# Performance work log

Hardware: AMD Instinct MI355X
Metric: run time of the kernel (lower is better)

Reference implementation:

```python
import jax, jax.numpy as jnp
import numpy as np

COMMITMENT_COST = 0.25
ENTROPY_LOSS_RATIO = 0.1
ENTROPY_TEMPERATURE = 0.01


def setup_inputs() -> dict:
    key = jax.random.key(0)
    k1, k2 = jax.random.split(key)
    x = jax.random.normal(k1, (64, 32, 32, 256), dtype=jnp.float32)
    # variance_scaling(fan_in, uniform) init for the codebook parameter
    codebook_size, emb_dim = 1024, 256
    limit = jnp.sqrt(3.0 / emb_dim)
    codebook = jax.random.uniform(k2, (codebook_size, emb_dim), jnp.float32, -limit, limit)
    return {"x": x, "codebook": codebook}


def _squared_euclidean_distance(a, b):
    # a: (n, d), b: (m, d) -> (n, m)
    a2 = jnp.sum(a * a, axis=1, keepdims=True)          # (n, 1)
    b2 = jnp.sum(b * b, axis=1)[None, :]                # (1, m)
    ab = jnp.matmul(a, b.T)                             # (n, m)
    return a2 - 2.0 * ab + b2


def _entropy_loss(affinity, temperature):
    # affinity: (..., K); loss_type='softmax'
    flat = affinity.reshape(-1, affinity.shape[-1]) / temperature
    probs = jax.nn.softmax(flat, axis=-1)
    log_probs = jax.nn.log_softmax(flat + 1e-05, axis=-1)
    target_probs = probs
    avg_probs = jnp.mean(target_probs, axis=0)
    avg_entropy = -jnp.sum(avg_probs * jnp.log(avg_probs + 1e-05))
    sample_entropy = -jnp.mean(jnp.sum(target_probs * log_probs, axis=-1))
    return sample_entropy - avg_entropy


def reference(x, codebook):
    sg = jax.lax.stop_gradient
    emb_dim = x.shape[-1]
    codebook_size = codebook.shape[0]
    flat_x = x.reshape(-1, emb_dim)                              # (N, d)
    distances = _squared_euclidean_distance(flat_x, codebook)    # (N, K)
    distances = distances.reshape(x.shape[:-1] + (codebook_size,))
    encoding_indices = jnp.argmin(distances, axis=-1)            # (B,H,W) int
    # quantize: onehot @ codebook == gather of codebook rows
    quantized = jnp.take(codebook, encoding_indices, axis=0)     # (B,H,W,d)

    e_latent_loss = jnp.mean((sg(quantized) - x) ** 2) * COMMITMENT_COST
    q_latent_loss = jnp.mean((quantized - sg(x)) ** 2)
    entropy_loss = _entropy_loss(-distances, ENTROPY_TEMPERATURE) * ENTROPY_LOSS_RATIO
    loss = (e_latent_loss + q_latent_loss + entropy_loss).astype(jnp.float32)

    # straight-through estimator
    quantized = x + sg(quantized - x)
    return quantized, loss, encoding_indices
```

## Files before the change

kernel.cpp:

```cpp
#include <hip/hip_runtime.h>
#include <math.h>

#define NROWS 65536
#define DIM   256
#define KCB   1024
#define TM    32
#define NBLK  (NROWS / TM)
#define QOFF  (NROWS * DIM)
#define IDXOFF (QOFF + 1)

#define WS_DMIN 0
#define WS_PLP  1
#define WS_AVGP 4
#define WS_C2   (WS_AVGP + 8 * 1024)
#define WS_CBF  (WS_C2 + 1024)

#define DELTA 0.05f
#define XBP   264

typedef __attribute__((ext_vector_type(8))) __bf16 bf16x8;
typedef __attribute__((ext_vector_type(4))) float  f32x4;
typedef __attribute__((ext_vector_type(8))) unsigned short u16x8;
typedef __attribute__((ext_vector_type(4))) unsigned short u16x4;

#define EP_REDD 0
#define EP_REDK 256
#define EP_RT1  512
#define EP_RT2  768
#define EP_GMIN 1024
#define EP_CNT  1056
#define EP_CAND 1088
#define EP_CEX  1600
#define EP_R1F  2112
#define EP_SP   2144
#define EP_KFIN 2176
#define EP_DFIN 2208
#define EP_AVGP 2240
#define EP_SIZE 3264

__device__ __forceinline__ unsigned short f2bf(float f) {
    unsigned u = __float_as_uint(f);
    u += 0x7fffu + ((u >> 16) & 1u);
    return (unsigned short)(u >> 16);
}

__global__ __launch_bounds__(256) void prep_kernel(const float* __restrict__ cb,
                                                   float* __restrict__ ws) {
    int gid = blockIdx.x * 256 + threadIdx.x;
    if (gid < 4) ws[gid] = 0.f;
    if (gid < 8192) ws[WS_AVGP + gid] = 0.f;

    int k  = gid >> 5;
    int s  = gid & 31;
    int kc = s >> 2;
    int qq = s & 3;

    if (gid < 1024) {
        const float4* row = (const float4*)(cb + (size_t)gid * DIM);
        float ssum = 0.f;
#pragma unroll 8
        for (int i = 0; i < DIM / 4; ++i) {
            float4 v = row[i];
            ssum += v.x * v.x + v.y * v.y + v.z * v.z + v.w * v.w;
        }
        ws[WS_C2 + gid] = ssum;
    }

    unsigned short* cbf = (unsigned short*)(ws + WS_CBF);
    const float* src = cb + (size_t)k * DIM + (kc << 5) + (qq << 3);
    float4 v0 = *(const float4*)src, v1 = *(const float4*)(src + 4);
    u16x8 o;
    o[0] = f2bf(v0.x); o[1] = f2bf(v0.y); o[2] = f2bf(v0.z); o[3] = f2bf(v0.w);
    o[4] = f2bf(v1.x); o[5] = f2bf(v1.y); o[6] = f2bf(v1.z); o[7] = f2bf(v1.w);
    *(u16x8*)(cbf + ((((size_t)(kc << 10) + k) << 2) + qq) * 8) = o;
}

__global__ __launch_bounds__(512, 4) void vq_main(const float* __restrict__ x,
                                                  const float* __restrict__ cb,
                                                  float* __restrict__ ws,
                                                  float* __restrict__ out) {
    __shared__ float epi[EP_SIZE];
    __shared__ unsigned short xs[32 * XBP];

    const int tid  = threadIdx.x;
    const int w    = tid >> 6;
    const int lane = tid & 63;
    const int m    = lane & 15;
    const int q    = lane >> 4;
    const int R0   = blockIdx.x * TM;

    const u16x8* cbf = (const u16x8*)(ws + WS_CBF);
    const u16x8* bbase = cbf + (((w << 6) + m) << 2) + q;

    u16x8 breg[2][4];
    bf16x8 ah[2];

    float4 t0 = *((const float4*)(x + (size_t)(R0 + (w << 2) + 0) * DIM) + lane);
    float4 t1 = *((const float4*)(x + (size_t)(R0 + (w << 2) + 1) * DIM) + lane);
    float4 t2 = *((const float4*)(x + (size_t)(R0 + (w << 2) + 2) * DIM) + lane);
    float4 t3 = *((const float4*)(x + (size_t)(R0 + (w << 2) + 3) * DIM) + lane);

    {
        const u16x8* p = bbase;
        breg[0][0] = p[0]; breg[0][1] = p[64]; breg[0][2] = p[128]; breg[0][3] = p[192];
    }

    {
        u16x4 o;
        o[0] = f2bf(t0.x); o[1] = f2bf(t0.y); o[2] = f2bf(t0.z); o[3] = f2bf(t0.w);
        *(u16x4*)(xs + ((w << 2) + 0) * XBP + (lane << 2)) = o;
        o[0] = f2bf(t1.x); o[1] = f2bf(t1.y); o[2] = f2bf(t1.z); o[3] = f2bf(t1.w);
        *(u16x4*)(xs + ((w << 2) + 1) * XBP + (lane << 2)) = o;
        o[0] = f2bf(t2.x); o[1] = f2bf(t2.y); o[2] = f2bf(t2.z); o[3] = f2bf(t2.w);
        *(u16x4*)(xs + ((w << 2) + 2) * XBP + (lane << 2)) = o;
        o[0] = f2bf(t3.x); o[1] = f2bf(t3.y); o[2] = f2bf(t3.z); o[3] = f2bf(t3.w);
        *(u16x4*)(xs + ((w << 2) + 3) * XBP + (lane << 2)) = o;
    }

    f32x4 acc[2][8];
#pragma unroll
    for (int a = 0; a < 2; ++a)
#pragma unroll
        for (int b = 0; b < 8; ++b) acc[a][b] = (f32x4)0.f;

    __syncthreads();

    ah[0] = __builtin_bit_cast(bf16x8, *(const u16x8*)(xs + m * XBP + (q << 3)));
    ah[1] = __builtin_bit_cast(bf16x8, *(const u16x8*)(xs + (16 + m) * XBP + (q << 3)));

#pragma unroll
    for (int sub = 0; sub < 16; ++sub) {
        const int pb = sub & 1;
        if (sub < 15) {
            const int ns = sub + 1;
            const u16x8* p = bbase + ((ns >> 1) << 12) + ((ns & 1) << 11);
            breg[pb ^ 1][0] = p[0];   breg[pb ^ 1][1] = p[64];
            breg[pb ^ 1][2] = p[128]; breg[pb ^ 1][3] = p[192];
        }
#pragma unroll
        for (int ct = 0; ct < 4; ++ct) {
            bf16x8 bh = __builtin_bit_cast(bf16x8, breg[pb][ct]);
            int cg = ((sub & 1) << 2) + ct;
            acc[0][cg] = __builtin_amdgcn_mfma_f32_16x16x32_bf16(ah[0], bh, acc[0][cg], 0, 0, 0);
            acc[1][cg] = __builtin_amdgcn_mfma_f32_16x16x32_bf16(ah[1], bh, acc[1][cg], 0, 0, 0);
        }
        if ((sub & 1) == 1 && sub < 15) {
            const int nkc = (sub >> 1) + 1;
            ah[0] = __builtin_bit_cast(bf16x8, *(const u16x8*)(xs + m * XBP + (nkc << 5) + (q << 3)));
            ah[1] = __builtin_bit_cast(bf16x8, *(const u16x8*)(xs + (16 + m) * XBP + (nkc << 5) + (q << 3)));
        }
    }

    if (tid < 32) ((int*)(epi + EP_CNT))[tid] = 0;
#pragma unroll
    for (int t = tid; t < 1024; t += 512) epi[EP_AVGP + t] = 0.f;

    float c2v[8];
#pragma unroll
    for (int cg = 0; cg < 8; ++cg) {
        int col = ((cg >> 2) << 9) + (w << 6) + ((cg & 3) << 4) + m;
        c2v[cg] = ws[WS_C2 + col];
    }
#pragma unroll
    for (int rt = 0; rt < 2; ++rt) {
#pragma unroll
        for (int reg = 0; reg < 4; ++reg) {
            int row = (rt << 4) + (q << 2) + reg;
            float md = 3.0e38f; int mk = 0;
#pragma unroll
            for (int cg = 0; cg < 8; ++cg) {
                float g = c2v[cg] - 2.0f * acc[rt][cg][reg];
                acc[rt][cg][reg] = g;
                int col = ((cg >> 2) << 9) + (w << 6) + ((cg & 3) << 4) + m;
                if (g < md) { md = g; mk = col; }
            }
#pragma unroll
            for (int off = 1; off <= 8; off <<= 1) {
                float od = __shfl_xor(md, off, 64);
                int   ok = __shfl_xor(mk, off, 64);
                if (od < md || (od == md && ok < mk)) { md = od; mk = ok; }
            }
            if (m == 0) {
                epi[EP_REDD + (w << 5) + row] = md;
                ((int*)(epi + EP_REDK))[(w << 5) + row] = mk;
            }
        }
    }
    __syncthreads();

    if (tid < 32) {
        float gm = 3.0e38f;
#pragma unroll
        for (int wv = 0; wv < 8; ++wv) {
            float d = epi[EP_REDD + (wv << 5) + tid];
            if (d < gm) gm = d;
        }
        epi[EP_GMIN + tid] = gm;
    }
    __syncthreads();

    {
        int* cnt  = (int*)(epi + EP_CNT);
        int* cand = (int*)(epi + EP_CAND);
#pragma unroll
        for (int rt = 0; rt < 2; ++rt) {
#pragma unroll
            for (int reg = 0; reg < 4; ++reg) {
                int row = (rt << 4) + (q << 2) + reg;
                float gm = epi[EP_GMIN + row];
                float t1 = 0.f, t2 = 0.f;
#pragma unroll
                for (int cg = 0; cg < 8; ++cg) {
                    float g = acc[rt][cg][reg];
                    if (g < gm + DELTA) {
                        int col = ((cg >> 2) << 9) + (w << 6) + ((cg & 3) << 4) + m;
                        int pos = atomicAdd(&cnt[row], 1);
                        if (pos < 16) cand[(row << 4) + pos] = col;
                    }
                    float z = -100.0f * (g - gm);
                    float e = __expf(z);
                    acc[rt][cg][reg] = e;
                    t1 += e;
                    t2 += e * z;
                }
#pragma unroll
                for (int off = 1; off <= 8; off <<= 1) {
                    t1 += __shfl_xor(t1, off, 64);
                    t2 += __shfl_xor(t2, off, 64);
                }
                if (m == 0) {
                    epi[EP_RT1 + (w << 5) + row] = t1;
                    epi[EP_RT2 + (w << 5) + row] = t2;
                }
            }
        }
    }
    __syncthreads();

    if (tid < 32) {
        float T1 = 0.f, T2 = 0.f;
#pragma unroll
        for (int wv = 0; wv < 8; ++wv) {
            T1 += epi[EP_RT1 + (wv << 5) + tid];
            T2 += epi[EP_RT2 + (wv << 5) + tid];
        }
        float r1 = 1.0f / T1;
        epi[EP_R1F + tid] = r1;
        epi[EP_SP + tid]  = T2 * r1 - logf(T1);
    }
    __syncthreads();

    {
        float r1v[2][4];
#pragma unroll
        for (int rt = 0; rt < 2; ++rt)
#pragma unroll
            for (int reg = 0; reg < 4; ++reg)
                r1v[rt][reg] = epi[EP_R1F + (rt << 4) + (q << 2) + reg];
#pragma unroll
        for (int cg = 0; cg < 8; ++cg) {
            float s = 0.f;
#pragma unroll
            for (int rt = 0; rt < 2; ++rt)
#pragma unroll
                for (int reg = 0; reg < 4; ++reg)
                    s += acc[rt][cg][reg] * r1v[rt][reg];
            s += __shfl_xor(s, 16, 64);
            s += __shfl_xor(s, 32, 64);
            if (lane < 16) {
                int col = ((cg >> 2) << 9) + (w << 6) + ((cg & 3) << 4) + m;
                epi[EP_AVGP + col] += s;
            }
        }
    }
    {
        int* cnt  = (int*)(epi + EP_CNT);
        int* cand = (int*)(epi + EP_CAND);
        int r = tid >> 4;
        int i = tid & 15;
        int n = cnt[r]; if (n > 16) n = 16;
        if (i < n) {
            int k = cand[(r << 4) + i];
            const float4* ax = (const float4*)(x  + (((size_t)(R0 + r)) << 8));
            const float4* bx = (const float4*)(cb + (((size_t)k) << 8));
            float ab = 0.f, x2 = 0.f;
#pragma unroll 8
            for (int d4 = 0; d4 < 64; ++d4) {
                float4 a = ax[d4], b = bx[d4];
                ab = fmaf(a.x, b.x, ab);
                ab = fmaf(a.y, b.y, ab);
                ab = fmaf(a.z, b.z, ab);
                ab = fmaf(a.w, b.w, ab);
                x2 += a.x * a.x + a.y * a.y + a.z * a.z + a.w * a.w;
            }
            float t = 2.0f * ab;
            epi[EP_CEX + (r << 4) + i] = (x2 - t) + ws[WS_C2 + k];
        }
    }
    __syncthreads();

    if (tid < 32) {
        int* cnt  = (int*)(epi + EP_CNT);
        int* cand = (int*)(epi + EP_CAND);
        int n = cnt[tid]; if (n > 16) n = 16;
        float bd = epi[EP_CEX + (tid << 4)];
        int   bk = cand[(tid << 4)];
        for (int i = 1; i < n; ++i) {
            float d = epi[EP_CEX + (tid << 4) + i];
            int   k = cand[(tid << 4) + i];
            if (d < bd || (d == bd && k < bk)) { bd = d; bk = k; }
        }
        ((int*)(epi + EP_KFIN))[tid] = bk;
        epi[EP_DFIN + tid] = bd;
        out[IDXOFF + R0 + tid] = (float)bk;
    }
    __syncthreads();

#pragma unroll
    for (int rr = 0; rr < 4; ++rr) {
        int r = (w << 2) + rr;
        int k = ((int*)(epi + EP_KFIN))[r];
        f32x4 v = *((const f32x4*)(cb + (((size_t)k) << 8)) + lane);
        __builtin_nontemporal_store(v, (f32x4*)(out + (((size_t)(R0 + r)) << 8)) + lane);
    }
    for (int t = tid; t < 1024; t += 512)
        atomicAdd(ws + WS_AVGP + ((blockIdx.x & 7) << 10) + t, epi[EP_AVGP + t]);
    if (tid < 32) {
        float sp = epi[EP_SP + tid];
        float dd = epi[EP_DFIN + tid];
#pragma unroll
        for (int off = 1; off <= 16; off <<= 1) {
            sp += __shfl_xor(sp, off, 64);
            dd += __shfl_xor(dd, off, 64);
        }
        if (tid == 0) {
            atomicAdd(ws + WS_PLP, sp);
            atomicAdd(ws + WS_DMIN, dd);
        }
    }
}

__global__ __launch_bounds__(256) void vq_finalize(const float* __restrict__ ws,
                                                   float* __restrict__ out) {
    __shared__ float red[4];
    int tid = threadIdx.x;
    float part = 0.f;
    for (int k = tid; k < 1024; k += 256) {
        float s = 0.f;
#pragma unroll
        for (int r = 0; r < 8; ++r) s += ws[WS_AVGP + (r << 10) + k];
        float ap = s * (1.0f / 65536.0f);
        part += ap * logf(ap + 1e-5f);
    }
#pragma unroll
    for (int off = 32; off; off >>= 1) part += __shfl_xor(part, off, 64);
    if ((tid & 63) == 0) red[tid >> 6] = part;
    __syncthreads();
    if (tid == 0) {
        float sum_aplog      = red[0] + red[1] + red[2] + red[3];
        float avg_entropy    = -sum_aplog;
        float sample_entropy = -ws[WS_PLP] * (1.0f / 65536.0f);
        float entropy_loss   = (sample_entropy - avg_entropy) * 0.1f;
        float eq = 1.25f * ws[WS_DMIN] * (1.0f / ((float)NROWS * (float)DIM));
        out[QOFF] = eq + entropy_loss;
    }
}

extern "C" void kernel_launch(void* const* d_in, const int* in_sizes, int n_in,
                              void* d_out, int out_size, void* d_ws, size_t ws_size,
                              hipStream_t stream) {
    const float* x  = (const float*)d_in[0];
    const float* cb = (const float*)d_in[1];
    float* out = (float*)d_out;
    float* ws  = (float*)d_ws;

    prep_kernel<<<128, 256, 0, stream>>>(cb, ws);
    vq_main<<<NBLK, 512, 0, stream>>>(x, cb, ws, out);
    vq_finalize<<<1, 256, 0, stream>>>(ws, out);
}
```

Measured before the change: 277.1 us.

## Stream codebook tiles into LDS via direct global-to-LDS loads with double buffering

The prep kernel now writes the bf16 codebook in a fragment-ordered layout, one contiguous 32KB chunk per k-sub-step. The main kernel pulls each chunk into a double-buffered LDS region with global_load_lds, replacing per-wave register prefetch of B fragments. The x tile is no longer staged in LDS but converted from fp32 to bf16 straight from global memory at each k chunk. The aim is to cut register pressure and redundant global B traffic, at the cost of a block-wide barrier every sub-step and extra LDS use (64KB for B) that may lower occupancy.

Measured after the change: 305.0 us. +10.1%, slower.

```diff
diff --git a/kernel.cpp b/kernel.cpp
--- a/kernel.cpp
+++ b/kernel.cpp
@@ -16,12 +16,10 @@
 #define WS_CBF  (WS_C2 + 1024)
 
 #define DELTA 0.05f
-#define XBP   264
 
 typedef __attribute__((ext_vector_type(8))) __bf16 bf16x8;
 typedef __attribute__((ext_vector_type(4))) float  f32x4;
 typedef __attribute__((ext_vector_type(8))) unsigned short u16x8;
-typedef __attribute__((ext_vector_type(4))) unsigned short u16x4;
 
 #define EP_REDD 0
 #define EP_REDK 256
@@ -44,6 +42,20 @@
     return (unsigned short)(u >> 16);
 }
 
+__device__ __forceinline__ bf16x8 cvt8(const float* src) {
+    float4 v0 = *(const float4*)src, v1 = *(const float4*)(src + 4);
+    u16x8 o;
+    o[0] = f2bf(v0.x); o[1] = f2bf(v0.y); o[2] = f2bf(v0.z); o[3] = f2bf(v0.w);
+    o[4] = f2bf(v1.x); o[5] = f2bf(v1.y); o[6] = f2bf(v1.z); o[7] = f2bf(v1.w);
+    return __builtin_bit_cast(bf16x8, o);
+}
+
+__device__ __forceinline__ void gload_lds16(const void* g, void* l) {
+    __builtin_amdgcn_global_load_lds(
+        (const __attribute__((address_space(1))) unsigned int*)g,
+        (__attribute__((address_space(3))) unsigned int*)l, 16, 0, 0);
+}
+
 __global__ __launch_bounds__(256) void prep_kernel(const float* __restrict__ cb,
                                                    float* __restrict__ ws) {
     int gid = blockIdx.x * 256 + threadIdx.x;
@@ -66,13 +78,20 @@
         ws[WS_C2 + gid] = ssum;
     }
 
+    int h  = k >> 9;
+    int wc = (k >> 6) & 7;
+    int ct = (k >> 4) & 3;
+    int m  = k & 15;
+    int sub = (kc << 1) + h;
+    size_t chunk = ((size_t)sub << 11) + (wc << 8) + (ct << 6) + (qq << 4) + m;
+
     unsigned short* cbf = (unsigned short*)(ws + WS_CBF);
     const float* src = cb + (size_t)k * DIM + (kc << 5) + (qq << 3);
     float4 v0 = *(const float4*)src, v1 = *(const float4*)(src + 4);
     u16x8 o;
     o[0] = f2bf(v0.x); o[1] = f2bf(v0.y); o[2] = f2bf(v0.z); o[3] = f2bf(v0.w);
     o[4] = f2bf(v1.x); o[5] = f2bf(v1.y); o[6] = f2bf(v1.z); o[7] = f2bf(v1.w);
-    *(u16x8*)(cbf + ((((size_t)(kc << 10) + k) << 2) + qq) * 8) = o;
+    *(u16x8*)(cbf + chunk * 8) = o;
 }
 
 __global__ __launch_bounds__(512, 4) void vq_main(const float* __restrict__ x,
@@ -80,7 +99,7 @@
                                                   float* __restrict__ ws,
                                                   float* __restrict__ out) {
     __shared__ float epi[EP_SIZE];
-    __shared__ unsigned short xs[32 * XBP];
+    __shared__ u16x8 ldsB[2][2048];
 
     const int tid  = threadIdx.x;
     const int w    = tid >> 6;
@@ -89,33 +108,21 @@
     const int q    = lane >> 4;
     const int R0   = blockIdx.x * TM;
 
-    const u16x8* cbf = (const u16x8*)(ws + WS_CBF);
-    const u16x8* bbase = cbf + (((w << 6) + m) << 2) + q;
-
-    u16x8 breg[2][4];
+    const char* gB = (const char*)(ws + WS_CBF);
+    const int fragoff = (w << 8) + lane;
+
     bf16x8 ah[2];
 
-    float4 t0 = *((const float4*)(x + (size_t)(R0 + (w << 2) + 0) * DIM) + lane);
-    float4 t1 = *((const float4*)(x + (size_t)(R0 + (w << 2) + 1) * DIM) + lane);
-    float4 t2 = *((const float4*)(x + (size_t)(R0 + (w << 2) + 2) * DIM) + lane);
-    float4 t3 = *((const float4*)(x + (size_t)(R0 + (w << 2) + 3) * DIM) + lane);
-
     {
-        const u16x8* p = bbase;
-        breg[0][0] = p[0]; breg[0][1] = p[64]; breg[0][2] = p[128]; breg[0][3] = p[192];
-    }
-
-    {
-        u16x4 o;
-        o[0] = f2bf(t0.x); o[1] = f2bf(t0.y); o[2] = f2bf(t0.z); o[3] = f2bf(t0.w);
-        *(u16x4*)(xs + ((w << 2) + 0) * XBP + (lane << 2)) = o;
-        o[0] = f2bf(t1.x); o[1] = f2bf(t1.y); o[2] = f2bf(t1.z); o[3] = f2bf(t1.w);
-        *(u16x4*)(xs + ((w << 2) + 1) * XBP + (lane << 2)) = o;
-        o[0] = f2bf(t2.x); o[1] = f2bf(t2.y); o[2] = f2bf(t2.z); o[3] = f2bf(t2.w);
-        *(u16x4*)(xs + ((w << 2) + 2) * XBP + (lane << 2)) = o;
-        o[0] = f2bf(t3.x); o[1] = f2bf(t3.y); o[2] = f2bf(t3.z); o[3] = f2bf(t3.w);
-        *(u16x4*)(xs + ((w << 2) + 3) * XBP + (lane << 2)) = o;
-    }
+        const char* g = gB + (size_t)tid * 16;
+        char* l = (char*)&ldsB[0][0] + (w << 10);
+        gload_lds16(g, l);
+        gload_lds16(g + 8192,  l + 8192);
+        gload_lds16(g + 16384, l + 16384);
+        gload_lds16(g + 24576, l + 24576);
+    }
+    ah[0] = cvt8(x + (size_t)(R0 + m) * DIM + (q << 3));
+    ah[1] = cvt8(x + (size_t)(R0 + 16 + m) * DIM + (q << 3));
 
     f32x4 acc[2][8];
 #pragma unroll
@@ -125,30 +132,33 @@
 
     __syncthreads();
 
-    ah[0] = __builtin_bit_cast(bf16x8, *(const u16x8*)(xs + m * XBP + (q << 3)));
-    ah[1] = __builtin_bit_cast(bf16x8, *(const u16x8*)(xs + (16 + m) * XBP + (q << 3)));
-
 #pragma unroll
     for (int sub = 0; sub < 16; ++sub) {
-        const int pb = sub & 1;
+        const int cur = sub & 1;
         if (sub < 15) {
-            const int ns = sub + 1;
-            const u16x8* p = bbase + ((ns >> 1) << 12) + ((ns & 1) << 11);
-            breg[pb ^ 1][0] = p[0];   breg[pb ^ 1][1] = p[64];
-            breg[pb ^ 1][2] = p[128]; breg[pb ^ 1][3] = p[192];
-        }
+            const char* g = gB + (size_t)(sub + 1) * 32768 + (size_t)tid * 16;
+            char* l = (char*)&ldsB[cur ^ 1][0] + (w << 10);
+            gload_lds16(g, l);
+            gload_lds16(g + 8192,  l + 8192);
+            gload_lds16(g + 16384, l + 16384);
+            gload_lds16(g + 24576, l + 24576);
+        }
+        const u16x8* lbc = &ldsB[cur][fragoff];
+        u16x8 f0 = lbc[0], f1 = lbc[64], f2 = lbc[128], f3 = lbc[192];
 #pragma unroll
         for (int ct = 0; ct < 4; ++ct) {
-            bf16x8 bh = __builtin_bit_cast(bf16x8, breg[pb][ct]);
+            u16x8 fr = (ct == 0) ? f0 : (ct == 1) ? f1 : (ct == 2) ? f2 : f3;
+            bf16x8 bh = __builtin_bit_cast(bf16x8, fr);
             int cg = ((sub & 1) << 2) + ct;
             acc[0][cg] = __builtin_amdgcn_mfma_f32_16x16x32_bf16(ah[0], bh, acc[0][cg], 0, 0, 0);
             acc[1][cg] = __builtin_amdgcn_mfma_f32_16x16x32_bf16(ah[1], bh, acc[1][cg], 0, 0, 0);
         }
         if ((sub & 1) == 1 && sub < 15) {
             const int nkc = (sub >> 1) + 1;
-            ah[0] = __builtin_bit_cast(bf16x8, *(const u16x8*)(xs + m * XBP + (nkc << 5) + (q << 3)));
-            ah[1] = __builtin_bit_cast(bf16x8, *(const u16x8*)(xs + (16 + m) * XBP + (nkc << 5) + (q << 3)));
-        }
+            ah[0] = cvt8(x + (size_t)(R0 + m) * DIM + (nkc << 5) + (q << 3));
+            ah[1] = cvt8(x + (size_t)(R0 + 16 + m) * DIM + (nkc << 5) + (q << 3));
+        }
+        if (sub < 15) __syncthreads();
     }
 
     if (tid < 32) ((int*)(epi + EP_CNT))[tid] = 0;
```
